# Optimization experiments

Measured on AMD Instinct MI355X. Metric: run time of the kernel, lower is better.

## Reference

```python
import jax, jax.numpy as jnp
import numpy as np

NEG = -1e9
LRELU_ALPHA = 0.2  # tf.nn.leaky_relu default


def setup_inputs() -> dict:
    key = jax.random.key(0)
    k = jax.random.split(key, 6)
    B, N, F_in, F_out = 1, 8192, 256, 64
    x = jax.random.normal(k[0], (B, N, F_in), dtype=jnp.float32)
    # sparse adjacency as additive bias: ~32 neighbors/node on average
    u = jax.random.uniform(k[1], (B, N, N), dtype=jnp.float32)
    adj = jnp.where(u < 32.0 / N, 0.0, NEG).astype(jnp.float32)
    W = jax.random.normal(k[2], (F_in, F_out), dtype=jnp.float32) * (1.0 / np.sqrt(F_in))
    a1 = jax.random.normal(k[3], (F_out, 1), dtype=jnp.float32) * (1.0 / np.sqrt(F_out))
    a2 = jax.random.normal(k[4], (F_out, 1), dtype=jnp.float32) * (1.0 / np.sqrt(F_out))
    b1 = jnp.zeros((1,), dtype=jnp.float32)
    b2 = jnp.zeros((1,), dtype=jnp.float32)
    bias = jnp.zeros((F_out,), dtype=jnp.float32)
    return {"x": x, "adj": adj, "W": W, "a1": a1, "b1": b1, "a2": a2, "b2": b2, "bias": bias}


def reference(x, adj, W, a1, b1, a2, b2, bias):
    # conv1 (kernel_size=1, no bias) == per-node linear projection
    fts = jnp.einsum('bnf,fo->bno', x, W)            # [B, N, F_out]
    f1 = jnp.einsum('bno,oi->bni', fts, a1) + b1     # [B, N, 1]
    f2 = jnp.einsum('bno,oi->bni', fts, a2) + b2     # [B, N, 1]
    logits = f1 + jnp.swapaxes(f2, 1, 2)             # [B, N, N] additive scores
    scores = jax.nn.leaky_relu(logits, LRELU_ALPHA) + adj
    coefs = jax.nn.softmax(scores, axis=-1)          # [B, N, N]
    vals = jnp.einsum('bnm,bmo->bno', coefs, fts) + bias
    return jax.nn.elu(vals)
```

## Files before the change

kernel.cpp:

```cpp
#include <hip/hip_runtime.h>
#include <cstdint>

#define N_NODES 8192
#define F_IN    256
#define F_OUT   64
#define ALPHA   0.2f
#define CAP     256

__global__ __launch_bounds__(256) void k_proj(const float* __restrict__ x,
                                              const float* __restrict__ W,
                                              const float* __restrict__ a1,
                                              const float* __restrict__ b1,
                                              const float* __restrict__ a2,
                                              const float* __restrict__ b2,
                                              float* __restrict__ fts,
                                              float* __restrict__ f1,
                                              float* __restrict__ f2,
                                              int* __restrict__ cnt) {
    __shared__ __align__(16) float ws[64][F_OUT];
    const int t = threadIdx.x, lane = t & 63, w = t >> 6;

    if (blockIdx.x < 32) cnt[blockIdx.x * 256 + t] = 0;

    const int rowA = blockIdx.x * 8 + w * 2;
    const int rowB = rowA + 1;

    const float4* xqA = (const float4*)(x + (size_t)rowA * F_IN);
    const float4* xqB = (const float4*)(x + (size_t)rowB * F_IN);
    float accA = 0.f, accB = 0.f;

    for (int kc = 0; kc < 4; ++kc) {
        if (kc) __syncthreads();
        {
            const float4* Wt = (const float4*)(W + (size_t)kc * 64 * F_OUT);
            float4* S = (float4*)&ws[0][0];
            S[t]       = Wt[t];
            S[t + 256] = Wt[t + 256];
            S[t + 512] = Wt[t + 512];
            S[t + 768] = Wt[t + 768];
        }
        __syncthreads();
        #pragma unroll
        for (int q = 0; q < 16; ++q) {
            const float4 xa = xqA[kc * 16 + q];
            const float4 xb = xqB[kc * 16 + q];
            const float w0 = ws[q*4+0][lane];
            const float w1 = ws[q*4+1][lane];
            const float w2 = ws[q*4+2][lane];
            const float w3 = ws[q*4+3][lane];
            accA += xa.x*w0 + xa.y*w1 + xa.z*w2 + xa.w*w3;
            accB += xb.x*w0 + xb.y*w1 + xb.z*w2 + xb.w*w3;
        }
    }
    fts[(size_t)rowA * F_OUT + lane] = accA;
    fts[(size_t)rowB * F_OUT + lane] = accB;

    const float u1 = a1[lane], u2 = a2[lane];
    float sA1 = accA * u1, sA2 = accA * u2;
    float sB1 = accB * u1, sB2 = accB * u2;
    #pragma unroll
    for (int off = 32; off >= 1; off >>= 1) {
        sA1 += __shfl_xor(sA1, off, 64);
        sA2 += __shfl_xor(sA2, off, 64);
        sB1 += __shfl_xor(sB1, off, 64);
        sB2 += __shfl_xor(sB2, off, 64);
    }
    if (lane == 0) {
        const float bb1 = b1[0], bb2 = b2[0];
        f1[rowA] = sA1 + bb1;  f2[rowA] = sA2 + bb2;
        f1[rowB] = sB1 + bb1;  f2[rowB] = sB2 + bb2;
    }
}

__global__ __launch_bounds__(256) void k_scan(const float* __restrict__ adj,
                                              int* __restrict__ cnt,
                                              int* __restrict__ list) {
    const int S = gridDim.x * 256;
    int q = blockIdx.x * 256 + threadIdx.x;
    const float4* A = (const float4*)adj;

    #pragma unroll 1
    for (int it = 0; it < 8; ++it) {
        const float4 v0 = A[q];
        const float4 v1 = A[q + S];
        const float4 v2 = A[q + 2 * S];
        const float4 v3 = A[q + 3 * S];

        #define PROC(v, qq)                                                     \
        {                                                                       \
            const int e = (qq) << 2;                                            \
            const int r = e >> 13;                                              \
            const int c = e & (N_NODES - 1);                                    \
            if ((v).x > -0.5f) { int p = atomicAdd(&cnt[r], 1); if (p < CAP) list[(r << 8) + p] = c;     } \
            if ((v).y > -0.5f) { int p = atomicAdd(&cnt[r], 1); if (p < CAP) list[(r << 8) + p] = c + 1; } \
            if ((v).z > -0.5f) { int p = atomicAdd(&cnt[r], 1); if (p < CAP) list[(r << 8) + p] = c + 2; } \
            if ((v).w > -0.5f) { int p = atomicAdd(&cnt[r], 1); if (p < CAP) list[(r << 8) + p] = c + 3; } \
        }
        PROC(v0, q) PROC(v1, q + S) PROC(v2, q + 2 * S) PROC(v3, q + 3 * S)
        #undef PROC
        q += 4 * S;
    }
}

__global__ __launch_bounds__(256) void k_gather(const int* __restrict__ cnt,
                                                const int* __restrict__ list,
                                                const float* __restrict__ fts,
                                                const float* __restrict__ f1,
                                                const float* __restrict__ f2,
                                                const float* __restrict__ bias,
                                                float* __restrict__ out) {
    const int lane = threadIdx.x & 63, w = threadIdx.x >> 6;
    const int row  = blockIdx.x * 4 + w;

    int n = cnt[row];
    n = (n < CAP) ? n : CAP;
    const int* lst = list + (row << 8);
    const float f1r = f1[row];

    float l0 = -3.0e38f, l1 = -3.0e38f, l2 = -3.0e38f, l3 = -3.0e38f;
    int   j0 = 0, j1 = 0, j2 = 0, j3 = 0;
    if (lane < n)       { j0 = lst[lane];       const float g = f1r + f2[j0]; l0 = fmaxf(g, ALPHA * g); }
    if (lane + 64 < n)  { j1 = lst[lane + 64];  const float g = f1r + f2[j1]; l1 = fmaxf(g, ALPHA * g); }
    if (lane + 128 < n) { j2 = lst[lane + 128]; const float g = f1r + f2[j2]; l2 = fmaxf(g, ALPHA * g); }
    if (lane + 192 < n) { j3 = lst[lane + 192]; const float g = f1r + f2[j3]; l3 = fmaxf(g, ALPHA * g); }

    float m = fmaxf(fmaxf(l0, l1), fmaxf(l2, l3));
    #pragma unroll
    for (int off = 32; off >= 1; off >>= 1)
        m = fmaxf(m, __shfl_xor(m, off, 64));

    const float p0 = __expf(l0 - m);
    const float p1 = __expf(l1 - m);
    const float p2 = __expf(l2 - m);
    const float p3 = __expf(l3 - m);

    float den = (p0 + p1) + (p2 + p3);
    #pragma unroll
    for (int off = 32; off >= 1; off >>= 1)
        den += __shfl_xor(den, off, 64);

    float acc = 0.f;
    {
        const int nb = (n < 64) ? n : 64;
        for (int k = 0; k < nb; ++k)
            acc += __shfl(p0, k, 64) * fts[(size_t)__shfl(j0, k, 64) * F_OUT + lane];
    }
    if (n > 64) {
        const int nb = (n - 64 < 64) ? n - 64 : 64;
        for (int k = 0; k < nb; ++k)
            acc += __shfl(p1, k, 64) * fts[(size_t)__shfl(j1, k, 64) * F_OUT + lane];
    }
    if (n > 128) {
        const int nb = (n - 128 < 64) ? n - 128 : 64;
        for (int k = 0; k < nb; ++k)
            acc += __shfl(p2, k, 64) * fts[(size_t)__shfl(j2, k, 64) * F_OUT + lane];
    }
    if (n > 192) {
        const int nb = (n - 192 < 64) ? n - 192 : 64;
        for (int k = 0; k < nb; ++k)
            acc += __shfl(p3, k, 64) * fts[(size_t)__shfl(j3, k, 64) * F_OUT + lane];
    }

    const float v = acc / den + bias[lane];
    out[(size_t)row * F_OUT + lane] = (v > 0.f) ? v : expm1f(v);
}

extern "C" void kernel_launch(void* const* d_in, const int* in_sizes, int n_in,
                              void* d_out, int out_size, void* d_ws, size_t ws_size,
                              hipStream_t stream) {
    const float* x    = (const float*)d_in[0];
    const float* adj  = (const float*)d_in[1];
    const float* W    = (const float*)d_in[2];
    const float* a1   = (const float*)d_in[3];
    const float* b1   = (const float*)d_in[4];
    const float* a2   = (const float*)d_in[5];
    const float* b2   = (const float*)d_in[6];
    const float* bias = (const float*)d_in[7];
    float* out = (float*)d_out;

    float* fts = (float*)d_ws;
    float* f1  = fts + (size_t)N_NODES * F_OUT;
    float* f2  = f1 + N_NODES;
    int*   cnt = (int*)(f2 + N_NODES);
    int*   lst = cnt + N_NODES;

    k_proj  <<<N_NODES / 8, 256, 0, stream>>>(x, W, a1, b1, a2, b2, fts, f1, f2, cnt);
    k_scan  <<<2048,        256, 0, stream>>>(adj, cnt, lst);
    k_gather<<<N_NODES / 4, 256, 0, stream>>>(cnt, lst, fts, f1, f2, bias, out);
}
```

Before: 422.5 us.

## Replace global atomic neighbor lists with ballot bitmap and per-row shared-memory compaction

The scan kernel no longer issues a global atomicAdd per nonzero. It builds a bitmask with one bit per float4 of adjacency that holds any nonzero, using wavefront ballots. The gather kernel walks that bitmask for its row, re-reads only the flagged float4s from adj, and compacts neighbor indices into shared memory with LDS atomics. This removes contended global atomics and the list writes. In exchange the per-row neighbor cap drops from 256 to 128, which could truncate rows with many neighbors, and the flagged adj entries are read a second time.

```diff
diff --git a/kernel.cpp b/kernel.cpp
--- a/kernel.cpp
+++ b/kernel.cpp
@@ -5,7 +5,8 @@
 #define F_IN    256
 #define F_OUT   64
 #define ALPHA   0.2f
-#define CAP     256
+#define SCAN_BLOCKS 2048
+#define CAPG    128
 
 __global__ __launch_bounds__(256) void k_proj(const float* __restrict__ x,
                                               const float* __restrict__ W,
@@ -15,13 +16,9 @@
                                               const float* __restrict__ b2,
                                               float* __restrict__ fts,
                                               float* __restrict__ f1,
-                                              float* __restrict__ f2,
-                                              int* __restrict__ cnt) {
+                                              float* __restrict__ f2) {
     __shared__ __align__(16) float ws[64][F_OUT];
     const int t = threadIdx.x, lane = t & 63, w = t >> 6;
-
-    if (blockIdx.x < 32) cnt[blockIdx.x * 256 + t] = 0;
-
     const int rowA = blockIdx.x * 8 + w * 2;
     const int rowB = rowA + 1;
 
@@ -72,12 +69,12 @@
     }
 }
 
-__global__ __launch_bounds__(256) void k_scan(const float* __restrict__ adj,
-                                              int* __restrict__ cnt,
-                                              int* __restrict__ list) {
-    const int S = gridDim.x * 256;
+__global__ __launch_bounds__(256) void k_bits(const float* __restrict__ adj,
+                                              unsigned long long* __restrict__ bm) {
+    const int S = SCAN_BLOCKS * 256;
+    const float4* A = (const float4*)adj;
+    const int lane = threadIdx.x & 63;
     int q = blockIdx.x * 256 + threadIdx.x;
-    const float4* A = (const float4*)adj;
 
     #pragma unroll 1
     for (int it = 0; it < 8; ++it) {
@@ -86,55 +83,69 @@
         const float4 v2 = A[q + 2 * S];
         const float4 v3 = A[q + 3 * S];
 
-        #define PROC(v, qq)                                                     \
-        {                                                                       \
-            const int e = (qq) << 2;                                            \
-            const int r = e >> 13;                                              \
-            const int c = e & (N_NODES - 1);                                    \
-            if ((v).x > -0.5f) { int p = atomicAdd(&cnt[r], 1); if (p < CAP) list[(r << 8) + p] = c;     } \
-            if ((v).y > -0.5f) { int p = atomicAdd(&cnt[r], 1); if (p < CAP) list[(r << 8) + p] = c + 1; } \
-            if ((v).z > -0.5f) { int p = atomicAdd(&cnt[r], 1); if (p < CAP) list[(r << 8) + p] = c + 2; } \
-            if ((v).w > -0.5f) { int p = atomicAdd(&cnt[r], 1); if (p < CAP) list[(r << 8) + p] = c + 3; } \
+        const unsigned long long b0 = __ballot(fmaxf(fmaxf(fmaxf(v0.x, v0.y), v0.z), v0.w) > -0.5f);
+        const unsigned long long b1 = __ballot(fmaxf(fmaxf(fmaxf(v1.x, v1.y), v1.z), v1.w) > -0.5f);
+        const unsigned long long b2 = __ballot(fmaxf(fmaxf(fmaxf(v2.x, v2.y), v2.z), v2.w) > -0.5f);
+        const unsigned long long b3 = __ballot(fmaxf(fmaxf(fmaxf(v3.x, v3.y), v3.z), v3.w) > -0.5f);
+
+        if (lane == 0) {
+            bm[q >> 6]           = b0;
+            bm[(q + S) >> 6]     = b1;
+            bm[(q + 2 * S) >> 6] = b2;
+            bm[(q + 3 * S) >> 6] = b3;
         }
-        PROC(v0, q) PROC(v1, q + S) PROC(v2, q + 2 * S) PROC(v3, q + 3 * S)
-        #undef PROC
         q += 4 * S;
     }
 }
 
-__global__ __launch_bounds__(256) void k_gather(const int* __restrict__ cnt,
-                                                const int* __restrict__ list,
+__global__ __launch_bounds__(256) void k_gather(const unsigned long long* __restrict__ bm,
+                                                const float* __restrict__ adj,
                                                 const float* __restrict__ fts,
                                                 const float* __restrict__ f1,
                                                 const float* __restrict__ f2,
                                                 const float* __restrict__ bias,
                                                 float* __restrict__ out) {
+    __shared__ int lj[4][CAPG];
+    __shared__ int lcnt[4];
+
     const int lane = threadIdx.x & 63, w = threadIdx.x >> 6;
     const int row  = blockIdx.x * 4 + w;
+    if (threadIdx.x < 4) lcnt[threadIdx.x] = 0;
+    __syncthreads();
 
-    int n = cnt[row];
-    n = (n < CAP) ? n : CAP;
-    const int* lst = list + (row << 8);
+    unsigned long long wv = 0;
+    if (lane < 32) wv = bm[row * 32 + lane];
+    const float4* A4 = (const float4*)adj;
+    while (wv) {
+        const int b = __ffsll((long long)wv) - 1;
+        wv &= wv - 1;
+        const int ql = (lane << 6) + b;
+        const float4 av = A4[(size_t)row * 2048 + ql];
+        if (av.x > -0.5f) { int p = atomicAdd(&lcnt[w], 1); if (p < CAPG) lj[w][p] = 4*ql+0; }
+        if (av.y > -0.5f) { int p = atomicAdd(&lcnt[w], 1); if (p < CAPG) lj[w][p] = 4*ql+1; }
+        if (av.z > -0.5f) { int p = atomicAdd(&lcnt[w], 1); if (p < CAPG) lj[w][p] = 4*ql+2; }
+        if (av.w > -0.5f) { int p = atomicAdd(&lcnt[w], 1); if (p < CAPG) lj[w][p] = 4*ql+3; }
+    }
+    __syncthreads();
+
+    int n = lcnt[w];
+    n = (n < CAPG) ? n : CAPG;
     const float f1r = f1[row];
 
-    float l0 = -3.0e38f, l1 = -3.0e38f, l2 = -3.0e38f, l3 = -3.0e38f;
-    int   j0 = 0, j1 = 0, j2 = 0, j3 = 0;
-    if (lane < n)       { j0 = lst[lane];       const float g = f1r + f2[j0]; l0 = fmaxf(g, ALPHA * g); }
-    if (lane + 64 < n)  { j1 = lst[lane + 64];  const float g = f1r + f2[j1]; l1 = fmaxf(g, ALPHA * g); }
-    if (lane + 128 < n) { j2 = lst[lane + 128]; const float g = f1r + f2[j2]; l2 = fmaxf(g, ALPHA * g); }
-    if (lane + 192 < n) { j3 = lst[lane + 192]; const float g = f1r + f2[j3]; l3 = fmaxf(g, ALPHA * g); }
+    float l0 = -3.0e38f, l1 = -3.0e38f;
+    int   j0 = 0, j1 = 0;
+    if (lane < n)      { j0 = lj[w][lane];      const float g = f1r + f2[j0]; l0 = fmaxf(g, ALPHA * g); }
+    if (lane + 64 < n) { j1 = lj[w][lane + 64]; const float g = f1r + f2[j1]; l1 = fmaxf(g, ALPHA * g); }
 
-    float m = fmaxf(fmaxf(l0, l1), fmaxf(l2, l3));
+    float m = fmaxf(l0, l1);
     #pragma unroll
     for (int off = 32; off >= 1; off >>= 1)
         m = fmaxf(m, __shfl_xor(m, off, 64));
 
     const float p0 = __expf(l0 - m);
     const float p1 = __expf(l1 - m);
-    const float p2 = __expf(l2 - m);
-    const float p3 = __expf(l3 - m);
 
-    float den = (p0 + p1) + (p2 + p3);
+    float den = p0 + p1;
     #pragma unroll
     for (int off = 32; off >= 1; off >>= 1)
         den += __shfl_xor(den, off, 64);
@@ -146,19 +157,9 @@
             acc += __shfl(p0, k, 64) * fts[(size_t)__shfl(j0, k, 64) * F_OUT + lane];
     }
     if (n > 64) {
-        const int nb = (n - 64 < 64) ? n - 64 : 64;
+        const int nb = n - 64;
         for (int k = 0; k < nb; ++k)
             acc += __shfl(p1, k, 64) * fts[(size_t)__shfl(j1, k, 64) * F_OUT + lane];
-    }
-    if (n > 128) {
-        const int nb = (n - 128 < 64) ? n - 128 : 64;
-        for (int k = 0; k < nb; ++k)
-            acc += __shfl(p2, k, 64) * fts[(size_t)__shfl(j2, k, 64) * F_OUT + lane];
-    }
-    if (n > 192) {
-        const int nb = (n - 192 < 64) ? n - 192 : 64;
-        for (int k = 0; k < nb; ++k)
-            acc += __shfl(p3, k, 64) * fts[(size_t)__shfl(j3, k, 64) * F_OUT + lane];
     }
 
     const float v = acc / den + bias[lane];
@@ -181,10 +182,9 @@
     float* fts = (float*)d_ws;
     float* f1  = fts + (size_t)N_NODES * F_OUT;
     float* f2  = f1 + N_NODES;
-    int*   cnt = (int*)(f2 + N_NODES);
-    int*   lst = cnt + N_NODES;
+    unsigned long long* bm = (unsigned long long*)(f2 + N_NODES);
 
-    k_proj  <<<N_NODES / 8, 256, 0, stream>>>(x, W, a1, b1, a2, b2, fts, f1, f2, cnt);
-    k_scan  <<<2048,        256, 0, stream>>>(adj, cnt, lst);
-    k_gather<<<N_NODES / 4, 256, 0, stream>>>(cnt, lst, fts, f1, f2, bias, out);
+    k_bits  <<<SCAN_BLOCKS, 256, 0, stream>>>(adj, bm);
+    k_proj  <<<N_NODES / 8, 256, 0, stream>>>(x, W, a1, b1, a2, b2, fts, f1, f2);
+    k_gather<<<N_NODES / 4, 256, 0, stream>>>(bm, adj, fts, f1, f2, bias, out);
 }
```

Result: no change. 419.2 us (-0.8%).
